# Kernel optimization log

Measured on AMD Instinct MI355X. Metric: run time of the kernel, lower is better.

Reference implementation:

```python
import jax, jax.numpy as jnp
import numpy as np

INPUT_DIM = 128
OUTPUT_DIM = 128
FEATURE_DIM = 2 * OUTPUT_DIM            # 256
EDGE_DIM = 2 * FEATURE_DIM              # 512
H_DIM = INPUT_DIM + FEATURE_DIM + 2 * EDGE_DIM  # input + xp + (mean,max) pooled
N_INTT = 50000
N_MVTX = 50000
N_EDGES = 320000


def _linear_params(key, fan_in, fan_out):
    kw, kb = jax.random.split(key)
    lim = 1.0 / np.sqrt(fan_in)
    W = jax.random.uniform(kw, (fan_in, fan_out), jnp.float32, -lim, lim)
    b = jax.random.uniform(kb, (fan_out,), jnp.float32, -lim, lim)
    return W, b


def setup_inputs() -> dict:
    key = jax.random.key(0)
    ks = jax.random.split(key, 10)
    x_intt = jax.random.normal(ks[0], (N_INTT, INPUT_DIM), jnp.float32)
    x_mvtx = jax.random.normal(ks[1], (N_MVTX, INPUT_DIM), jnp.float32)
    start = jax.random.randint(ks[2], (N_EDGES,), 0, N_INTT)
    end = jax.random.randint(ks[3], (N_EDGES,), 0, N_MVTX)
    edge_index = jnp.stack([start, end], axis=0).astype(jnp.int64) if jax.config.jax_enable_x64 else jnp.stack([start, end], axis=0)
    W_in_intt, b_in_intt = _linear_params(ks[4], INPUT_DIM, FEATURE_DIM)
    W_in_mvtx, b_in_mvtx = _linear_params(ks[5], INPUT_DIM, FEATURE_DIM)
    W_score, b_score = _linear_params(ks[6], EDGE_DIM, 1)
    W_out_intt, b_out_intt = _linear_params(ks[7], H_DIM, OUTPUT_DIM)
    W_out_mvtx, b_out_mvtx = _linear_params(ks[8], H_DIM, OUTPUT_DIM)
    return {
        "x_intt": x_intt, "x_mvtx": x_mvtx, "edge_index": edge_index,
        "W_in_intt": W_in_intt, "b_in_intt": b_in_intt,
        "W_in_mvtx": W_in_mvtx, "b_in_mvtx": b_in_mvtx,
        "W_score": W_score, "b_score": b_score,
        "W_out_intt": W_out_intt, "b_out_intt": b_out_intt,
        "W_out_mvtx": W_out_mvtx, "b_out_mvtx": b_out_mvtx,
    }


def _scatter_mean(edges, idx, n):
    # torch_scatter.scatter_mean with out=zeros: sum / max(count, 1)
    s = jax.ops.segment_sum(edges, idx, num_segments=n)
    cnt = jax.ops.segment_sum(jnp.ones((edges.shape[0], 1), edges.dtype), idx, num_segments=n)
    return s / jnp.maximum(cnt, 1.0)


def _scatter_max(edges, idx, n):
    # torch_scatter.scatter_max with out=zeros: out participates in the max -> clamp at 0
    m = jax.ops.segment_max(edges, idx, num_segments=n)
    return jnp.maximum(m, 0.0)


def reference(x_intt, x_mvtx, edge_index,
              W_in_intt, b_in_intt, W_in_mvtx, b_in_mvtx,
              W_score, b_score, W_out_intt, b_out_intt,
              W_out_mvtx, b_out_mvtx):
    xp_intt = x_intt @ W_in_intt + b_in_intt          # [Ni, F]
    xp_mvtx = x_mvtx @ W_in_mvtx + b_in_mvtx          # [Nm, F]
    start, end = edge_index[0], edge_index[1]
    xp = jnp.concatenate([xp_intt[start], xp_mvtx[end]], axis=-1)  # [E, 2F]
    # aggregator_activation = 'potential': exp(-|x|)
    score = jnp.exp(-jnp.abs(xp @ W_score + b_score))  # [E, 1]
    edges = xp * score                                 # [E, 2F]

    mean_intt = _scatter_mean(edges, start, x_intt.shape[0])
    max_intt = _scatter_max(edges, start, x_intt.shape[0])
    mean_mvtx = _scatter_mean(edges, end, x_mvtx.shape[0])
    max_mvtx = _scatter_max(edges, end, x_mvtx.shape[0])

    H_intt = jnp.concatenate([x_intt, xp_intt, mean_intt, max_intt], axis=-1)
    H_mvtx = jnp.concatenate([x_mvtx, xp_mvtx, mean_mvtx, max_mvtx], axis=-1)
    h_intt = jax.nn.relu(H_intt @ W_out_intt + b_out_intt)
    h_mvtx = jax.nn.relu(H_mvtx @ W_out_mvtx + b_out_mvtx)
    return (h_intt, h_mvtx)
```

## Files before the change

### kernel.cpp

```cpp
#include <hip/hip_runtime.h>


typedef __attribute__((ext_vector_type(8))) short bf16x8;
typedef __attribute__((ext_vector_type(4))) float f32x4;

static __device__ __forceinline__ unsigned short f2bf(float f) {
  unsigned int u = __float_as_uint(f);
  u = (u + 0x7FFFu + ((u >> 16) & 1u)) >> 16;
  return (unsigned short)u;
}
static __device__ __forceinline__ float bf2f(unsigned short s) {
  return __uint_as_float(((unsigned int)s) << 16);
}

#define GLD16(gp, lp)                                                        \
  __builtin_amdgcn_global_load_lds(                                          \
      (const __attribute__((address_space(1))) void*)(gp),                   \
      (__attribute__((address_space(3))) void*)(lp), 16, 0, 0)

__global__ void k_prep_wt(const float* __restrict__ Wo,
                          unsigned short* __restrict__ Wt, int K, int Ncol) {
  int idx = blockIdx.x * blockDim.x + threadIdx.x;
  if (idx >= K * Ncol) return;
  int k = idx / Ncol, c = idx % Ncol;
  Wt[(size_t)c * K + k] = f2bf(Wo[idx]);
}

__global__ __launch_bounds__(256) void k_gemm_in(
    const float* __restrict__ x, const unsigned short* __restrict__ Wint,
    const float* __restrict__ bias, const float* __restrict__ Wsc,
    unsigned short* __restrict__ xp, float* __restrict__ a_out, int N) {
  __shared__ __align__(16) unsigned short Ab[64 * 16 * 8];
  __shared__ __align__(16) unsigned short Bb[256 * 16 * 8];
  const int tid = threadIdx.x;
  const int l = tid & 63;
  const int lr = l & 15, lg = l >> 4;
  const int w = tid >> 6, wr = w >> 1, wc = w & 1;
  const int r0 = blockIdx.x * 64;
  const int wbase = tid & 192;

#pragma unroll
  for (int i = 0; i < 16; ++i) {
    int g = i * 256 + tid;
    int row = g >> 4, c = g & 15;
    int sc = c ^ (row & 7);
    GLD16(Wint + (size_t)row * 128 + sc * 8,
          &Bb[(size_t)(i * 256 + wbase) * 8]);
  }
#pragma unroll
  for (int i = 0; i < 4; ++i) {
    int g = i * 256 + tid;
    int row = g >> 4, c = g & 15;
    int ar = min(r0 + row, N - 1);
    const float* src = x + (size_t)ar * 128 + c * 8;
    float4 u = *(const float4*)src;
    float4 v = *(const float4*)(src + 4);
    bf16x8 h;
    h[0] = (short)f2bf(u.x); h[1] = (short)f2bf(u.y);
    h[2] = (short)f2bf(u.z); h[3] = (short)f2bf(u.w);
    h[4] = (short)f2bf(v.x); h[5] = (short)f2bf(v.y);
    h[6] = (short)f2bf(v.z); h[7] = (short)f2bf(v.w);
    *(bf16x8*)&Ab[(size_t)(row * 16 + (c ^ (row & 7))) * 8] = h;
  }
  __syncthreads();

  f32x4 acc[2][8];
#pragma unroll
  for (int m = 0; m < 2; ++m)
#pragma unroll
    for (int t = 0; t < 8; ++t) {
      f32x4 z = {0.f, 0.f, 0.f, 0.f};
      acc[m][t] = z;
    }
#pragma unroll
  for (int kk = 0; kk < 4; ++kk) {
    int chq = kk * 4 + lg;
    bf16x8 a[2], bt[8];
#pragma unroll
    for (int m = 0; m < 2; ++m) {
      int row = wr * 32 + m * 16 + lr;
      a[m] = *(const bf16x8*)&Ab[(row * 16 + (chq ^ (row & 7))) * 8];
    }
#pragma unroll
    for (int t = 0; t < 8; ++t) {
      int row = wc * 128 + t * 16 + lr;
      bt[t] = *(const bf16x8*)&Bb[(row * 16 + (chq ^ (row & 7))) * 8];
    }
#pragma unroll
    for (int m = 0; m < 2; ++m)
#pragma unroll
      for (int t = 0; t < 8; ++t)
        acc[m][t] = __builtin_amdgcn_mfma_f32_16x16x32_bf16(
            a[m], bt[t], acc[m][t], 0, 0, 0);
  }

  float wscv[8], bb[8];
#pragma unroll
  for (int t = 0; t < 8; ++t) {
    int c = wc * 128 + t * 16 + lr;
    wscv[t] = Wsc[c];
    bb[t] = bias[c];
  }
#pragma unroll
  for (int m = 0; m < 2; ++m) {
    int rb = r0 + wr * 32 + m * 16 + lg * 4;
    float p0 = 0.f, p1 = 0.f, p2 = 0.f, p3 = 0.f;
#pragma unroll
    for (int t = 0; t < 8; ++t) {
      int c = wc * 128 + t * 16 + lr;
      float v0 = acc[m][t][0] + bb[t];
      float v1 = acc[m][t][1] + bb[t];
      float v2 = acc[m][t][2] + bb[t];
      float v3 = acc[m][t][3] + bb[t];
      if (rb + 0 < N) xp[(size_t)(rb + 0) * 256 + c] = f2bf(v0);
      if (rb + 1 < N) xp[(size_t)(rb + 1) * 256 + c] = f2bf(v1);
      if (rb + 2 < N) xp[(size_t)(rb + 2) * 256 + c] = f2bf(v2);
      if (rb + 3 < N) xp[(size_t)(rb + 3) * 256 + c] = f2bf(v3);
      p0 = fmaf(v0, wscv[t], p0); p1 = fmaf(v1, wscv[t], p1);
      p2 = fmaf(v2, wscv[t], p2); p3 = fmaf(v3, wscv[t], p3);
    }
#pragma unroll
    for (int off = 1; off < 16; off <<= 1) {
      p0 += __shfl_xor(p0, off); p1 += __shfl_xor(p1, off);
      p2 += __shfl_xor(p2, off); p3 += __shfl_xor(p3, off);
    }
    if (lr == 0) {
      if (rb + 0 < N) atomicAdd(a_out + rb + 0, p0);
      if (rb + 1 < N) atomicAdd(a_out + rb + 1, p1);
      if (rb + 2 < N) atomicAdd(a_out + rb + 2, p2);
      if (rb + 3 < N) atomicAdd(a_out + rb + 3, p3);
    }
  }
}

__global__ void k_deg(const int* __restrict__ es, const int* __restrict__ ee,
                      int E, int* __restrict__ deg_i, int* __restrict__ deg_m) {
  int e = blockIdx.x * blockDim.x + threadIdx.x;
  if (e >= E) return;
  atomicAdd(deg_i + es[e], 1);
  atomicAdd(deg_m + ee[e], 1);
}

__global__ __launch_bounds__(256) void k_scan_blk(
    const int* __restrict__ deg, int* __restrict__ blksum, int n) {
  __shared__ int sm[256];
  int t = threadIdx.x;
  int i = blockIdx.x * 256 + t;
  sm[t] = (i < n) ? deg[i] : 0;
  __syncthreads();
#pragma unroll
  for (int off = 128; off; off >>= 1) {
    if (t < off) sm[t] += sm[t + off];
    __syncthreads();
  }
  if (t == 0) blksum[blockIdx.x] = sm[0];
}

__global__ __launch_bounds__(1024) void k_scan_top(
    const int* __restrict__ bs_i, int* __restrict__ bb_i, int nbi,
    const int* __restrict__ bs_m, int* __restrict__ bb_m, int nbm) {
  const int* bs = blockIdx.x ? bs_m : bs_i;
  int* bb = blockIdx.x ? bb_m : bb_i;
  int nb = blockIdx.x ? nbm : nbi;
  __shared__ int sm[1024];
  int t = threadIdx.x;
  int d = (t < nb) ? bs[t] : 0;
  sm[t] = d;
  __syncthreads();
  for (int off = 1; off < 1024; off <<= 1) {
    int v = (t >= off) ? sm[t - off] : 0;
    __syncthreads();
    sm[t] += v;
    __syncthreads();
  }
  if (t < nb) bb[t] = sm[t] - d;
}

__global__ __launch_bounds__(256) void k_scan_wr(
    const int* __restrict__ deg, const int* __restrict__ blkbase,
    int* __restrict__ rp, int* __restrict__ cur, int n, int E) {
  __shared__ int sm[256];
  int t = threadIdx.x;
  int i = blockIdx.x * 256 + t;
  int d = (i < n) ? deg[i] : 0;
  sm[t] = d;
  __syncthreads();
  for (int off = 1; off < 256; off <<= 1) {
    int v = (t >= off) ? sm[t - off] : 0;
    __syncthreads();
    sm[t] += v;
    __syncthreads();
  }
  if (i < n) {
    int v = blkbase[blockIdx.x] + sm[t] - d;
    rp[i] = v; cur[i] = v;
  }
  if (i == 0) rp[n] = E;
}

__global__ void k_fill(const int* __restrict__ es, const int* __restrict__ ee,
                       int E, const float* __restrict__ a_i,
                       const float* __restrict__ a_m,
                       const float* __restrict__ bsc,
                       int* __restrict__ cur_i, int* __restrict__ col_i,
                       float* __restrict__ sv_i,
                       int* __restrict__ cur_m, int* __restrict__ col_m,
                       float* __restrict__ sv_m) {
  int e = blockIdx.x * blockDim.x + threadIdx.x;
  if (e >= E) return;
  int s = es[e], m = ee[e];
  float sc = expf(-fabsf(a_i[s] + a_m[m] + bsc[0]));
  int pi = atomicAdd(cur_i + s, 1);
  col_i[pi] = m; sv_i[pi] = sc;
  int pm = atomicAdd(cur_m + m, 1);
  col_m[pm] = s; sv_m[pm] = sc;
}

__global__ __launch_bounds__(256) void k_agg(
    const unsigned short* __restrict__ xp_oth,
    const int* __restrict__ rowptr, const int* __restrict__ col,
    const float* __restrict__ sv, unsigned short* __restrict__ Hg,
    float4* __restrict__ scal, int base, int cnt) {
  int local = blockIdx.x * 4 + (threadIdx.x >> 6);
  if (local >= cnt) return;
  int node = base + local;
  int l = threadIdx.x & 63;

  float sum_s = 0.f, mx_s = -1e30f, mn_s = 1e30f;
  float sv0 = 0.f, sv1 = 0.f, sv2 = 0.f, sv3 = 0.f;
  float mv0 = -1e30f, mv1 = -1e30f, mv2 = -1e30f, mv3 = -1e30f;
  int jb = rowptr[node], je = rowptr[node + 1];
  int dg = je - jb;
  int j = jb;
  for (; j + 3 < je; j += 4) {
    int o0 = col[j], o1 = col[j + 1], o2 = col[j + 2], o3 = col[j + 3];
    float s0 = sv[j], s1 = sv[j + 1], s2 = sv[j + 2], s3 = sv[j + 3];
    ushort4 g0 = *(const ushort4*)(xp_oth + (size_t)o0 * 256 + 4 * l);
    ushort4 g1 = *(const ushort4*)(xp_oth + (size_t)o1 * 256 + 4 * l);
    ushort4 g2 = *(const ushort4*)(xp_oth + (size_t)o2 * 256 + 4 * l);
    ushort4 g3 = *(const ushort4*)(xp_oth + (size_t)o3 * 256 + 4 * l);
    float f0, f1, f2, f3;
    f0 = bf2f(g0.x); f1 = bf2f(g0.y); f2 = bf2f(g0.z); f3 = bf2f(g0.w);
    sv0 = fmaf(s0, f0, sv0); sv1 = fmaf(s0, f1, sv1);
    sv2 = fmaf(s0, f2, sv2); sv3 = fmaf(s0, f3, sv3);
    mv0 = fmaxf(mv0, s0 * f0); mv1 = fmaxf(mv1, s0 * f1);
    mv2 = fmaxf(mv2, s0 * f2); mv3 = fmaxf(mv3, s0 * f3);
    f0 = bf2f(g1.x); f1 = bf2f(g1.y); f2 = bf2f(g1.z); f3 = bf2f(g1.w);
    sv0 = fmaf(s1, f0, sv0); sv1 = fmaf(s1, f1, sv1);
    sv2 = fmaf(s1, f2, sv2); sv3 = fmaf(s1, f3, sv3);
    mv0 = fmaxf(mv0, s1 * f0); mv1 = fmaxf(mv1, s1 * f1);
    mv2 = fmaxf(mv2, s1 * f2); mv3 = fmaxf(mv3, s1 * f3);
    f0 = bf2f(g2.x); f1 = bf2f(g2.y); f2 = bf2f(g2.z); f3 = bf2f(g2.w);
    sv0 = fmaf(s2, f0, sv0); sv1 = fmaf(s2, f1, sv1);
    sv2 = fmaf(s2, f2, sv2); sv3 = fmaf(s2, f3, sv3);
    mv0 = fmaxf(mv0, s2 * f0); mv1 = fmaxf(mv1, s2 * f1);
    mv2 = fmaxf(mv2, s2 * f2); mv3 = fmaxf(mv3, s2 * f3);
    f0 = bf2f(g3.x); f1 = bf2f(g3.y); f2 = bf2f(g3.z); f3 = bf2f(g3.w);
    sv0 = fmaf(s3, f0, sv0); sv1 = fmaf(s3, f1, sv1);
    sv2 = fmaf(s3, f2, sv2); sv3 = fmaf(s3, f3, sv3);
    mv0 = fmaxf(mv0, s3 * f0); mv1 = fmaxf(mv1, s3 * f1);
    mv2 = fmaxf(mv2, s3 * f2); mv3 = fmaxf(mv3, s3 * f3);
    sum_s += (s0 + s1) + (s2 + s3);
    mx_s = fmaxf(mx_s, fmaxf(fmaxf(s0, s1), fmaxf(s2, s3)));
    mn_s = fminf(mn_s, fminf(fminf(s0, s1), fminf(s2, s3)));
  }
  for (; j < je; ++j) {
    int o0 = col[j];
    float s0 = sv[j];
    ushort4 g0 = *(const ushort4*)(xp_oth + (size_t)o0 * 256 + 4 * l);
    float f0 = bf2f(g0.x), f1 = bf2f(g0.y), f2 = bf2f(g0.z), f3 = bf2f(g0.w);
    sv0 = fmaf(s0, f0, sv0); sv1 = fmaf(s0, f1, sv1);
    sv2 = fmaf(s0, f2, sv2); sv3 = fmaf(s0, f3, sv3);
    mv0 = fmaxf(mv0, s0 * f0); mv1 = fmaxf(mv1, s0 * f1);
    mv2 = fmaxf(mv2, s0 * f2); mv3 = fmaxf(mv3, s0 * f3);
    sum_s += s0; mx_s = fmaxf(mx_s, s0); mn_s = fminf(mn_s, s0);
  }
  float inv = 1.f / (float)(dg > 0 ? dg : 1);
  unsigned short* Hr = Hg + (size_t)local * 512;
  *(ushort4*)(Hr + 4 * l) = make_ushort4(
      f2bf(sv0 * inv), f2bf(sv1 * inv), f2bf(sv2 * inv), f2bf(sv3 * inv));
  *(ushort4*)(Hr + 256 + 4 * l) = make_ushort4(
      f2bf(fmaxf(mv0, 0.f)), f2bf(fmaxf(mv1, 0.f)),
      f2bf(fmaxf(mv2, 0.f)), f2bf(fmaxf(mv3, 0.f)));
  if (l == 0)
    scal[local] = make_float4(sum_s * inv, dg > 0 ? mx_s : 0.f,
                              dg > 0 ? mn_s : 0.f, 0.f);
}

__global__ __launch_bounds__(512) void k_gemm_out(
    const float* __restrict__ x, const unsigned short* __restrict__ xp,
    const unsigned short* __restrict__ Hg, const float4* __restrict__ scal,
    const unsigned short* __restrict__ Wt, const float* __restrict__ bias,
    float* __restrict__ out, int Nloc, int own_first) {
  __shared__ unsigned short Ab[2][128 * 64];
  __shared__ unsigned short Bb[2][128 * 64];
  const int tid = threadIdx.x;
  const int l = tid & 63;
  const int lr = l & 15, lg = l >> 4;
  const int w = tid >> 6;
  const int wr = w >> 1, wc = w & 1;
  const int r0 = blockIdx.x * 128;
  const int wbase = tid & 448;

  int arw[2], acl[2], ar[2], asc[2];
  size_t adst[2];
  float ssv[2], mxv[2], mnv[2];
#pragma unroll
  for (int i = 0; i < 2; ++i) {
    int g = i * 512 + tid;
    arw[i] = g >> 3; acl[i] = g & 7;
    ar[i] = min(r0 + arw[i], Nloc - 1);
    asc[i] = acl[i] ^ (arw[i] & 7);
    adst[i] = (size_t)(arw[i] * 8 + asc[i]) * 8;
    float4 s4 = scal[ar[i]];
    ssv[i] = s4.x; mxv[i] = s4.y; mnv[i] = s4.z;
  }

  f32x4 acc[2][4];
#pragma unroll
  for (int m = 0; m < 2; ++m)
#pragma unroll
    for (int t = 0; t < 4; ++t) {
      f32x4 z = {0.f, 0.f, 0.f, 0.f};
      acc[m][t] = z;
    }

  auto stage = [&](int b, int t) {
#pragma unroll
    for (int i = 0; i < 2; ++i) {
      if (t < 2) {
        const float* src = x + (size_t)ar[i] * 128 + t * 64 + acl[i] * 8;
        float4 u = *(const float4*)src;
        float4 v = *(const float4*)(src + 4);
        bf16x8 h;
        h[0] = (short)f2bf(u.x); h[1] = (short)f2bf(u.y);
        h[2] = (short)f2bf(u.z); h[3] = (short)f2bf(u.w);
        h[4] = (short)f2bf(v.x); h[5] = (short)f2bf(v.y);
        h[6] = (short)f2bf(v.z); h[7] = (short)f2bf(v.w);
        *(bf16x8*)&Ab[b][adst[i]] = h;
      } else if (t < 6) {
        GLD16(xp + (size_t)ar[i] * 256 + (t - 2) * 64 + asc[i] * 8,
              &Ab[b][(size_t)(i * 512 + wbase) * 8]);
      } else {
        int phase = (t - 6) >> 2, sub = (t - 6) & 3;
        int is_own = own_first ? !(phase & 1) : (phase & 1);
        if (is_own) {
          bf16x8 v =
              *(const bf16x8*)(xp + (size_t)ar[i] * 256 + sub * 64 + acl[i] * 8);
          bf16x8 h;
          if (phase < 2) {
#pragma unroll
            for (int q = 0; q < 8; ++q)
              h[q] = (short)f2bf(bf2f((unsigned short)v[q]) * ssv[i]);
          } else {
#pragma unroll
            for (int q = 0; q < 8; ++q) {
              float f = bf2f((unsigned short)v[q]);
              h[q] = (short)f2bf(fmaxf(fmaxf(f * mxv[i], f * mnv[i]), 0.f));
            }
          }
          *(bf16x8*)&Ab[b][adst[i]] = h;
        } else {
          int hoff = (phase >= 2 ? 256 : 0) + sub * 64;
          GLD16(Hg + (size_t)ar[i] * 512 + hoff + asc[i] * 8,
                &Ab[b][(size_t)(i * 512 + wbase) * 8]);
        }
      }
    }
    int kb = t * 64;
#pragma unroll
    for (int i = 0; i < 2; ++i) {
      int g = i * 512 + tid;
      int row = g >> 3, c = g & 7;
      int sc = c ^ (row & 7);
      GLD16(Wt + (size_t)row * 1408 + kb + sc * 8,
            &Bb[b][(size_t)(i * 512 + wbase) * 8]);
    }
  };

  auto compute = [&](int b) {
#pragma unroll
    for (int kk = 0; kk < 2; ++kk) {
      int chq = kk * 4 + lg;
      bf16x8 a[2], bt[4];
#pragma unroll
      for (int m = 0; m < 2; ++m) {
        int row = wr * 32 + m * 16 + lr;
        a[m] = *(const bf16x8*)&Ab[b][(row * 8 + (chq ^ (row & 7))) * 8];
      }
#pragma unroll
      for (int t = 0; t < 4; ++t) {
        int row = wc * 64 + t * 16 + lr;
        bt[t] = *(const bf16x8*)&Bb[b][(row * 8 + (chq ^ (row & 7))) * 8];
      }
#pragma unroll
      for (int m = 0; m < 2; ++m)
#pragma unroll
        for (int t = 0; t < 4; ++t)
          acc[m][t] = __builtin_amdgcn_mfma_f32_16x16x32_bf16(
              a[m], bt[t], acc[m][t], 0, 0, 0);
    }
  };

  stage(0, 0);
  __syncthreads();
  int cur = 0;
  for (int t = 0; t < 22; ++t) {
    if (t < 21) stage(cur ^ 1, t + 1);
    compute(cur);
    __syncthreads();
    cur ^= 1;
  }

#pragma unroll
  for (int m = 0; m < 2; ++m) {
    int rb = r0 + wr * 32 + m * 16 + lg * 4;
#pragma unroll
    for (int t = 0; t < 4; ++t) {
      int c = wc * 64 + t * 16 + lr;
      float bbias = bias[c];
#pragma unroll
      for (int r = 0; r < 4; ++r) {
        int rr = rb + r;
        if (rr < Nloc) out[(size_t)rr * 128 + c] = fmaxf(acc[m][t][r] + bbias, 0.f);
      }
    }
  }
}

extern "C" void kernel_launch(void* const* d_in, const int* in_sizes, int n_in,
                              void* d_out, int out_size, void* d_ws,
                              size_t ws_size, hipStream_t stream) {
  const float* x_i  = (const float*)d_in[0];
  const float* x_m  = (const float*)d_in[1];
  const int*   ei   = (const int*)d_in[2];
  const float* Wi_i = (const float*)d_in[3];
  const float* bi_i = (const float*)d_in[4];
  const float* Wi_m = (const float*)d_in[5];
  const float* bi_m = (const float*)d_in[6];
  const float* Wsc  = (const float*)d_in[7];
  const float* bsc  = (const float*)d_in[8];
  const float* Wo_i = (const float*)d_in[9];
  const float* bo_i = (const float*)d_in[10];
  const float* Wo_m = (const float*)d_in[11];
  const float* bo_m = (const float*)d_in[12];
  float* out = (float*)d_out;

  int Ni = in_sizes[0] / 128, Nm = in_sizes[1] / 128, E = in_sizes[2] / 2;
  const int* es = ei;
  const int* ee = ei + E;
  int nbi = (Ni + 255) / 256, nbm = (Nm + 255) / 256;

  char* p = (char*)d_ws;
  auto alloc = [&](size_t bytes) {
    char* q = p;
    p += (bytes + 255) & ~(size_t)255;
    return q;
  };
  unsigned short* xp_i = (unsigned short*)alloc((size_t)Ni * 256 * 2);
  unsigned short* xp_m = (unsigned short*)alloc((size_t)Nm * 256 * 2);
  float* a_i   = (float*)alloc((size_t)Ni * 4);
  float* a_m   = (float*)alloc((size_t)Nm * 4);
  int* deg_i   = (int*)alloc((size_t)Ni * 4);
  int* deg_m   = (int*)alloc((size_t)Nm * 4);
  int* rp_i    = (int*)alloc((size_t)(Ni + 1) * 4);
  int* rp_m    = (int*)alloc((size_t)(Nm + 1) * 4);
  int* cur_i   = (int*)alloc((size_t)Ni * 4);
  int* cur_m   = (int*)alloc((size_t)Nm * 4);
  int* bs_i    = (int*)alloc((size_t)nbi * 4);
  int* bs_m    = (int*)alloc((size_t)nbm * 4);
  int* bb_i    = (int*)alloc((size_t)nbi * 4);
  int* bb_m    = (int*)alloc((size_t)nbm * 4);
  int* col_i   = (int*)alloc((size_t)E * 4);
  int* col_m   = (int*)alloc((size_t)E * 4);
  float* sv_i  = (float*)alloc((size_t)E * 4);
  float* sv_m  = (float*)alloc((size_t)E * 4);
  unsigned short* Wt_i = (unsigned short*)alloc((size_t)128 * 1408 * 2);
  unsigned short* Wt_m = (unsigned short*)alloc((size_t)128 * 1408 * 2);
  unsigned short* Wint_i = (unsigned short*)alloc((size_t)256 * 128 * 2);
  unsigned short* Wint_m = (unsigned short*)alloc((size_t)256 * 128 * 2);

  size_t used = (size_t)(p - (char*)d_ws);
  if (used + 256 > ws_size) return;
  size_t avail = ws_size - used - 256;
  long long srows_ll = (long long)(avail / 1040);
  int maxN = (Ni > Nm ? Ni : Nm);
  int maxPad = (maxN + 127) & ~127;
  int S = (int)(srows_ll > maxPad ? maxPad : srows_ll);
  S &= ~127;
  if (S < 128) return;
  unsigned short* Hg = (unsigned short*)alloc((size_t)S * 512 * 2);
  float4* scal = (float4*)alloc((size_t)S * 16);

  hipMemsetAsync(deg_i, 0, (size_t)Ni * 4, stream);
  hipMemsetAsync(deg_m, 0, (size_t)Nm * 4, stream);
  hipMemsetAsync(a_i, 0, (size_t)Ni * 4, stream);
  hipMemsetAsync(a_m, 0, (size_t)Nm * 4, stream);

  k_prep_wt<<<(1408 * 128 + 255) / 256, 256, 0, stream>>>(Wo_i, Wt_i, 1408, 128);
  k_prep_wt<<<(1408 * 128 + 255) / 256, 256, 0, stream>>>(Wo_m, Wt_m, 1408, 128);
  k_prep_wt<<<(128 * 256 + 255) / 256, 256, 0, stream>>>(Wi_i, Wint_i, 128, 256);
  k_prep_wt<<<(128 * 256 + 255) / 256, 256, 0, stream>>>(Wi_m, Wint_m, 128, 256);

  k_gemm_in<<<(Ni + 63) / 64, 256, 0, stream>>>(x_i, Wint_i, bi_i, Wsc, xp_i, a_i, Ni);
  k_gemm_in<<<(Nm + 63) / 64, 256, 0, stream>>>(x_m, Wint_m, bi_m, Wsc + 256, xp_m, a_m, Nm);

  k_deg<<<(E + 255) / 256, 256, 0, stream>>>(es, ee, E, deg_i, deg_m);
  k_scan_blk<<<nbi, 256, 0, stream>>>(deg_i, bs_i, Ni);
  k_scan_blk<<<nbm, 256, 0, stream>>>(deg_m, bs_m, Nm);
  k_scan_top<<<2, 1024, 0, stream>>>(bs_i, bb_i, nbi, bs_m, bb_m, nbm);
  k_scan_wr<<<nbi, 256, 0, stream>>>(deg_i, bb_i, rp_i, cur_i, Ni, E);
  k_scan_wr<<<nbm, 256, 0, stream>>>(deg_m, bb_m, rp_m, cur_m, Nm, E);
  k_fill<<<(E + 255) / 256, 256, 0, stream>>>(es, ee, E, a_i, a_m, bsc,
                                              cur_i, col_i, sv_i,
                                              cur_m, col_m, sv_m);

  for (int base = 0; base < Ni; base += S) {
    int cnt = Ni - base; if (cnt > S) cnt = S;
    k_agg<<<(cnt + 3) / 4, 256, 0, stream>>>(xp_m, rp_i, col_i, sv_i,
                                             Hg, scal, base, cnt);
    k_gemm_out<<<(cnt + 127) / 128, 512, 0, stream>>>(
        x_i + (size_t)base * 128, xp_i + (size_t)base * 256, Hg, scal,
        Wt_i, bo_i, out + (size_t)base * 128, cnt, 1);
  }
  float* out_m = out + (size_t)Ni * 128;
  for (int base = 0; base < Nm; base += S) {
    int cnt = Nm - base; if (cnt > S) cnt = S;
    k_agg<<<(cnt + 3) / 4, 256, 0, stream>>>(xp_i, rp_m, col_m, sv_m,
                                             Hg, scal, base, cnt);
    k_gemm_out<<<(cnt + 127) / 128, 512, 0, stream>>>(
        x_m + (size_t)base * 128, xp_m + (size_t)base * 256, Hg, scal,
        Wt_m, bo_m, out_m + (size_t)base * 128, cnt, 0);
  }
}
```

Before: 275.3 us.

## Pipeline output GEMM with prefetch distance two and explicit vmcnt waits

Restructures the output GEMM main loop into a two-stage-ahead software pipeline. Register loads for tile t+2 are issued before computing tile t, and the LDS writes and global-to-LDS loads are issued after a barrier. Partial s_waitcnt vmcnt counts replace the full __syncthreads drain. The own-first flag becomes a template parameter so the per-tile type branches resolve at compile time. The intent is to hide global load latency behind MFMA work. The hand-counted vmcnt values are fragile and could give races if the compiler reorders or adds memory operations.

Measured after the change: 272.4 us. No clear change (-1.0%).

```diff
diff --git a/kernel.cpp b/kernel.cpp
--- a/kernel.cpp
+++ b/kernel.cpp
@@ -287,11 +287,12 @@
                               dg > 0 ? mn_s : 0.f, 0.f);
 }
 
+template <int OWN_FIRST>
 __global__ __launch_bounds__(512) void k_gemm_out(
     const float* __restrict__ x, const unsigned short* __restrict__ xp,
     const unsigned short* __restrict__ Hg, const float4* __restrict__ scal,
     const unsigned short* __restrict__ Wt, const float* __restrict__ bias,
-    float* __restrict__ out, int Nloc, int own_first) {
+    float* __restrict__ out, int Nloc) {
   __shared__ unsigned short Ab[2][128 * 64];
   __shared__ unsigned short Bb[2][128 * 64];
   const int tid = threadIdx.x;
@@ -316,56 +317,54 @@
     ssv[i] = s4.x; mxv[i] = s4.y; mnv[i] = s4.z;
   }
 
-  f32x4 acc[2][4];
-#pragma unroll
-  for (int m = 0; m < 2; ++m)
-#pragma unroll
-    for (int t = 0; t < 4; ++t) {
-      f32x4 z = {0.f, 0.f, 0.f, 0.f};
-      acc[m][t] = z;
-    }
-
-  auto stage = [&](int b, int t) {
-#pragma unroll
-    for (int i = 0; i < 2; ++i) {
-      if (t < 2) {
+  auto ptype = [](int t) -> int {
+    if (t < 2) return 0;
+    if (t < 6) return 1;
+    int phase = (t - 6) >> 2;
+    int own = OWN_FIRST ? !(phase & 1) : (phase & 1);
+    return own ? 2 : 3;
+  };
+  auto gcnt = [&](int t) -> int {
+    if (t > 21) return 0;
+    int pt = ptype(t);
+    return (pt == 1 || pt == 3) ? 4 : 2;
+  };
+
+  float4 px4[2][2];
+  bf16x8 pxp[2];
+
+  auto stage_regload = [&](int t) {
+    int pt = ptype(t);
+    if (pt == 0) {
+#pragma unroll
+      for (int i = 0; i < 2; ++i) {
         const float* src = x + (size_t)ar[i] * 128 + t * 64 + acl[i] * 8;
-        float4 u = *(const float4*)src;
-        float4 v = *(const float4*)(src + 4);
-        bf16x8 h;
-        h[0] = (short)f2bf(u.x); h[1] = (short)f2bf(u.y);
-        h[2] = (short)f2bf(u.z); h[3] = (short)f2bf(u.w);
-        h[4] = (short)f2bf(v.x); h[5] = (short)f2bf(v.y);
-        h[6] = (short)f2bf(v.z); h[7] = (short)f2bf(v.w);
-        *(bf16x8*)&Ab[b][adst[i]] = h;
-      } else if (t < 6) {
+        px4[i][0] = *(const float4*)src;
+        px4[i][1] = *(const float4*)(src + 4);
+      }
+    } else if (pt == 2) {
+      int sub = (t - 6) & 3;
+#pragma unroll
+      for (int i = 0; i < 2; ++i)
+        pxp[i] = *(const bf16x8*)(xp + (size_t)ar[i] * 256 + sub * 64 +
+                                  acl[i] * 8);
+    }
+  };
+
+  auto stage_gld = [&](int t, int b) {
+    int pt = ptype(t);
+    if (pt == 1) {
+#pragma unroll
+      for (int i = 0; i < 2; ++i)
         GLD16(xp + (size_t)ar[i] * 256 + (t - 2) * 64 + asc[i] * 8,
               &Ab[b][(size_t)(i * 512 + wbase) * 8]);
-      } else {
-        int phase = (t - 6) >> 2, sub = (t - 6) & 3;
-        int is_own = own_first ? !(phase & 1) : (phase & 1);
-        if (is_own) {
-          bf16x8 v =
-              *(const bf16x8*)(xp + (size_t)ar[i] * 256 + sub * 64 + acl[i] * 8);
-          bf16x8 h;
-          if (phase < 2) {
-#pragma unroll
-            for (int q = 0; q < 8; ++q)
-              h[q] = (short)f2bf(bf2f((unsigned short)v[q]) * ssv[i]);
-          } else {
-#pragma unroll
-            for (int q = 0; q < 8; ++q) {
-              float f = bf2f((unsigned short)v[q]);
-              h[q] = (short)f2bf(fmaxf(fmaxf(f * mxv[i], f * mnv[i]), 0.f));
-            }
-          }
-          *(bf16x8*)&Ab[b][adst[i]] = h;
-        } else {
-          int hoff = (phase >= 2 ? 256 : 0) + sub * 64;
-          GLD16(Hg + (size_t)ar[i] * 512 + hoff + asc[i] * 8,
-                &Ab[b][(size_t)(i * 512 + wbase) * 8]);
-        }
-      }
+    } else if (pt == 3) {
+      int phase = (t - 6) >> 2, sub = (t - 6) & 3;
+      int hoff = (phase >= 2 ? 256 : 0) + sub * 64;
+#pragma unroll
+      for (int i = 0; i < 2; ++i)
+        GLD16(Hg + (size_t)ar[i] * 512 + hoff + asc[i] * 8,
+              &Ab[b][(size_t)(i * 512 + wbase) * 8]);
     }
     int kb = t * 64;
 #pragma unroll
@@ -378,6 +377,48 @@
     }
   };
 
+  auto stage_write = [&](int t, int b) {
+    int pt = ptype(t);
+    if (pt == 0) {
+#pragma unroll
+      for (int i = 0; i < 2; ++i) {
+        bf16x8 h;
+        h[0] = (short)f2bf(px4[i][0].x); h[1] = (short)f2bf(px4[i][0].y);
+        h[2] = (short)f2bf(px4[i][0].z); h[3] = (short)f2bf(px4[i][0].w);
+        h[4] = (short)f2bf(px4[i][1].x); h[5] = (short)f2bf(px4[i][1].y);
+        h[6] = (short)f2bf(px4[i][1].z); h[7] = (short)f2bf(px4[i][1].w);
+        *(bf16x8*)&Ab[b][adst[i]] = h;
+      }
+    } else if (pt == 2) {
+      int phase = (t - 6) >> 2;
+#pragma unroll
+      for (int i = 0; i < 2; ++i) {
+        bf16x8 h;
+        if (phase < 2) {
+#pragma unroll
+          for (int q = 0; q < 8; ++q)
+            h[q] = (short)f2bf(bf2f((unsigned short)pxp[i][q]) * ssv[i]);
+        } else {
+#pragma unroll
+          for (int q = 0; q < 8; ++q) {
+            float f = bf2f((unsigned short)pxp[i][q]);
+            h[q] = (short)f2bf(fmaxf(fmaxf(f * mxv[i], f * mnv[i]), 0.f));
+          }
+        }
+        *(bf16x8*)&Ab[b][adst[i]] = h;
+      }
+    }
+  };
+
+  f32x4 acc[2][4];
+#pragma unroll
+  for (int m = 0; m < 2; ++m)
+#pragma unroll
+    for (int t = 0; t < 4; ++t) {
+      f32x4 z = {0.f, 0.f, 0.f, 0.f};
+      acc[m][t] = z;
+    }
+
   auto compute = [&](int b) {
 #pragma unroll
     for (int kk = 0; kk < 2; ++kk) {
@@ -402,15 +443,33 @@
     }
   };
 
-  stage(0, 0);
-  __syncthreads();
-  int cur = 0;
+  auto wait_cnt = [&](int n) {
+    if (n >= 4)
+      asm volatile("s_waitcnt vmcnt(4) lgkmcnt(0)" ::: "memory");
+    else if (n >= 2)
+      asm volatile("s_waitcnt vmcnt(2) lgkmcnt(0)" ::: "memory");
+    else
+      asm volatile("s_waitcnt vmcnt(0) lgkmcnt(0)" ::: "memory");
+  };
+
+  stage_regload(0); stage_gld(0, 0); stage_write(0, 0);
+  stage_regload(1); stage_gld(1, 1); stage_write(1, 1);
+
   for (int t = 0; t < 22; ++t) {
-    if (t < 21) stage(cur ^ 1, t + 1);
-    compute(cur);
-    __syncthreads();
-    cur ^= 1;
-  }
+    int b = t & 1;
+    wait_cnt(gcnt(t + 1));
+    __builtin_amdgcn_s_barrier();
+    __builtin_amdgcn_sched_barrier(0);
+    if (t + 2 <= 21) stage_regload(t + 2);
+    compute(b);
+    __builtin_amdgcn_s_barrier();
+    __builtin_amdgcn_sched_barrier(0);
+    if (t + 2 <= 21) {
+      stage_gld(t + 2, b);
+      stage_write(t + 2, b);
+    }
+  }
+  asm volatile("s_waitcnt vmcnt(0) lgkmcnt(0)" ::: "memory");
 
 #pragma unroll
   for (int m = 0; m < 2; ++m) {
@@ -519,17 +578,17 @@
     int cnt = Ni - base; if (cnt > S) cnt = S;
     k_agg<<<(cnt + 3) / 4, 256, 0, stream>>>(xp_m, rp_i, col_i, sv_i,
                                              Hg, scal, base, cnt);
-    k_gemm_out<<<(cnt + 127) / 128, 512, 0, stream>>>(
+    k_gemm_out<1><<<(cnt + 127) / 128, 512, 0, stream>>>(
         x_i + (size_t)base * 128, xp_i + (size_t)base * 256, Hg, scal,
-        Wt_i, bo_i, out + (size_t)base * 128, cnt, 1);
+        Wt_i, bo_i, out + (size_t)base * 128, cnt);
   }
   float* out_m = out + (size_t)Ni * 128;
   for (int base = 0; base < Nm; base += S) {
     int cnt = Nm - base; if (cnt > S) cnt = S;
     k_agg<<<(cnt + 3) / 4, 256, 0, stream>>>(xp_i, rp_m, col_m, sv_m,
                                              Hg, scal, base, cnt);
-    k_gemm_out<<<(cnt + 127) / 128, 512, 0, stream>>>(
+    k_gemm_out<0><<<(cnt + 127) / 128, 512, 0, stream>>>(
         x_m + (size_t)base * 128, xp_m + (size_t)base * 256, Hg, scal,
-        Wt_m, bo_m, out_m + (size_t)base * 128, cnt, 0);
-  }
-}
+        Wt_m, bo_m, out_m + (size_t)base * 128, cnt);
+  }
+}
```
